# Performance work log

Measured on AMD Instinct MI355X. Metric: run time of the kernel, lower is better.

## Reference

```python
import jax, jax.numpy as jnp
import numpy as np

# dims: T time steps, B batch, CIN/COUT conv channels, HxW spatial, K kernel
T, B, CIN, COUT, H, Wd, K = 10, 32, 3, 64, 64, 64, 3
DECAY = 0.2      # LIF leak factor
INH = 1.625      # lateral inhibition strength (mode='threshold')


def setup_inputs() -> dict:
    key = jax.random.key(0)
    k1, k2 = jax.random.split(key)
    x = (jax.random.uniform(k1, (T, B, CIN, H, Wd)) < 0.2).astype(jnp.float32)
    W = jax.random.normal(k2, (COUT, CIN, K, K), dtype=jnp.float32)
    # normweight(): zero-mean, unit-std (biased) per output filter
    W = W - W.mean(axis=(1, 2, 3), keepdims=True)
    W = W / W.reshape(COUT, -1).std(axis=1).reshape(COUT, 1, 1, 1)
    return {"x": x, "W": W}


def _conv(x, W):
    # Conv2d stride=1, padding=1, no bias, NCHW/OIHW
    return jax.lax.conv_general_dilated(
        x, W, window_strides=(1, 1), padding=((1, 1), (1, 1)),
        dimension_numbers=("NCHW", "OIHW", "NCHW"))


def reference(x, W):
    def step(mem, x_t):
        i = _conv(x_t, W)                                        # (B,COUT,H,W)
        # ATB: adaptive per-channel threshold = max over batch+spatial
        thr = jnp.max(i, axis=(0, 2, 3), keepdims=True) + 1e-4   # (1,COUT,1,1)
        # ASF: clamp then thresholded sigmoid filter
        cur = jnp.maximum(i, 0.0)
        i_asf = thr * jax.nn.sigmoid((cur - 0.4 * thr) * (8.0 / thr))
        # LIF update with threshold = thr (set by ATB)
        mem = mem * DECAY + i_asf
        s = (mem > thr).astype(mem.dtype)                        # spikes 0/1
        # WTA k=1: keep only the strongest spiking channel per location
        score = mem * s
        winner = jnp.argmax(score, axis=1)                       # (B,H,W)
        oh = jnp.moveaxis(jax.nn.one_hot(winner, COUT, dtype=mem.dtype), -1, 1)
        s = s * oh
        # membrane reset of fired neurons
        mem = mem * (1.0 - s)
        # lateral inhibition: suppress non-winners at spiking locations
        any_sp = jnp.max(s, axis=1, keepdims=True)
        mem = mem - INH * thr * any_sp * (1.0 - s)
        return mem, s

    mem0 = jnp.zeros((B, COUT, H, Wd), jnp.float32)
    _, spikes = jax.lax.scan(step, mem0, x)
    return spikes  # (T,B,COUT,H,W)
```

## Files before the change

kernel.cpp:

```cpp
#include <hip/hip_runtime.h>
#include <math.h>

#define TT 10
#define BB 32
#define CIN 3
#define COUT 64
#define HH 64
#define WW 64
#define HW (HH*WW)
#define DECAY 0.2f
#define INH 1.625f

__device__ __forceinline__ unsigned int enc_f(float f) {
    unsigned int u = __float_as_uint(f);
    return (u & 0x80000000u) ? ~u : (u | 0x80000000u);
}
__device__ __forceinline__ float dec_f(unsigned int u) {
    u = (u & 0x80000000u) ? (u & 0x7FFFFFFFu) : ~u;
    return __uint_as_float(u);
}

__global__ __launch_bounds__(256) void thr_kernel(
    const float* __restrict__ x,
    const float* __restrict__ Wt,
    unsigned int* __restrict__ thr_raw)
{
    __shared__ float sx[CIN][6][68];
    __shared__ float wmax[4][COUT];

    const int tid  = threadIdx.x;
    const int lane = tid & 63;
    const int wave = tid >> 6;
    const int h0   = blockIdx.x * 4;
    const int b    = blockIdx.y;
    const int t    = blockIdx.z;

    float w[27];
    #pragma unroll
    for (int k = 0; k < 27; k++) w[k] = Wt[lane * 27 + k];

    const float* xb = x + ((size_t)t * BB + b) * (CIN * HW);
    for (int l = tid; l < CIN * 6 * 66; l += 256) {
        int ci  = l / 396;
        int r   = (l % 396) / 66;
        int col = l % 66;
        int gh = h0 + r - 1;
        int gw = col - 1;
        float v = 0.f;
        if (gh >= 0 && gh < HH && gw >= 0 && gw < WW)
            v = xb[ci * HW + gh * WW + gw];
        sx[ci][r][col] = v;
    }
    __syncthreads();

    float mx = -INFINITY;

    for (int cc = 0; cc < 16; cc++) {
        float acc0 = 0.f, acc1 = 0.f, acc2 = 0.f, acc3 = 0.f;
        #pragma unroll
        for (int ci = 0; ci < CIN; ci++)
            #pragma unroll
            for (int kh = 0; kh < 3; kh++) {
                const float* rp = &sx[ci][wave + kh][cc * 4];
                float4 q = *(const float4*)rp;
                float2 r2 = *(const float2*)(rp + 4);
                float x0 = q.x, x1 = q.y, x2 = q.z, x3 = q.w;
                float x4 = r2.x, x5 = r2.y;
                const float w0 = w[ci * 9 + kh * 3 + 0];
                const float w1 = w[ci * 9 + kh * 3 + 1];
                const float w2 = w[ci * 9 + kh * 3 + 2];
                acc0 = fmaf(w0, x0, acc0); acc0 = fmaf(w1, x1, acc0); acc0 = fmaf(w2, x2, acc0);
                acc1 = fmaf(w0, x1, acc1); acc1 = fmaf(w1, x2, acc1); acc1 = fmaf(w2, x3, acc1);
                acc2 = fmaf(w0, x2, acc2); acc2 = fmaf(w1, x3, acc2); acc2 = fmaf(w2, x4, acc2);
                acc3 = fmaf(w0, x3, acc3); acc3 = fmaf(w1, x4, acc3); acc3 = fmaf(w2, x5, acc3);
            }
        mx = fmaxf(mx, fmaxf(fmaxf(acc0, acc1), fmaxf(acc2, acc3)));
    }

    wmax[wave][lane] = mx;
    __syncthreads();
    if (wave == 0) {
        float m = fmaxf(fmaxf(wmax[0][lane], wmax[1][lane]),
                        fmaxf(wmax[2][lane], wmax[3][lane]));
        atomicMax(&thr_raw[t * COUT + lane], enc_f(m));
    }
}

__global__ __launch_bounds__(256) void fused_kernel(
    const float* __restrict__ x,
    const float* __restrict__ Wt,
    const unsigned int* __restrict__ thr_raw,
    float* __restrict__ out)
{
    __shared__ float sx[CIN][3][68];

    const int tid  = threadIdx.x;
    const int lane = tid & 63;
    const int wave = tid >> 6;
    const int p0   = __builtin_amdgcn_readfirstlane(wave * 16);
    const int b    = blockIdx.x >> 6;
    const int h    = blockIdx.x & 63;

    float w[27];
    #pragma unroll
    for (int k = 0; k < 27; k++) w[k] = Wt[lane * 27 + k];

    float mem[16];
    #pragma unroll
    for (int j = 0; j < 16; j++) mem[j] = 0.f;

    #pragma unroll 1
    for (int t = 0; t < TT; t++) {
        const float* xb = x + ((size_t)t * BB + b) * (CIN * HW);
        for (int l = tid; l < CIN * 3 * 66; l += 256) {
            int ci  = l / 198;
            int r   = (l % 198) / 66;
            int col = l % 66;
            int gh = h + r - 1;
            int gw = col - 1;
            float v = 0.f;
            if (gh >= 0 && gh < HH && gw >= 0 && gw < WW)
                v = xb[ci * HW + gh * WW + gw];
            sx[ci][r][col] = v;
        }

        float* os = out + (((size_t)t * BB + b) * COUT) * HW + h * WW;

        #pragma unroll
        for (int g = 0; g < 4; g++) {
            int c  = g * 16 + (tid >> 4);
            int w4 = (tid & 15) * 4;
            *(float4*)(os + (size_t)c * HW + w4) = make_float4(0.f, 0.f, 0.f, 0.f);
        }

        __syncthreads();

        float thr   = dec_f(thr_raw[t * COUT + lane]) + 1e-4f;
        float sinv  = 8.0f / thr;
        float s04   = 0.4f * thr;
        float sinh_ = INH * thr;

        int fmask = 0;

#define LIF_PX(J, ACC) {                                                    \
        float cur = fmaxf(ACC, 0.f);                                        \
        float z   = (cur - s04) * sinv;                                     \
        float sig = 1.0f / (1.0f + expf(-z));                               \
        float m   = mem[J] * DECAY + thr * sig;                             \
        int   sp  = m > thr;                                                \
        float score = sp ? m : 0.f;                                         \
        unsigned long long blt = __ballot(sp);                              \
        int fr = 0, sp_any = 0;                                             \
        if (blt) {                                  \
            float bs = score;                                               \
            int   bc = lane;                                                \
            _Pragma("unroll")                                               \
            for (int off = 32; off > 0; off >>= 1) {                        \
                float so = __shfl_xor(bs, off, 64);                         \
                int   co = __shfl_xor(bc, off, 64);                         \
                if (so > bs || (so == bs && co < bc)) { bs = so; bc = co; } \
            }                                                               \
            int spw = __shfl(sp, bc, 64);      \
            fr     = (lane == bc) && sp;                                    \
            sp_any = spw;                                                   \
        }                                                                   \
        mem[J] = fr ? 0.f : (m - (sp_any ? sinh_ : 0.f));                   \
        if (fr) fmask |= (1 << (J));                                        \
    }

        #pragma unroll
        for (int ch = 0; ch < 4; ch++) {
            const int c0 = p0 + ch * 4;
            float acc0 = 0.f, acc1 = 0.f, acc2 = 0.f, acc3 = 0.f;
            #pragma unroll
            for (int ci = 0; ci < CIN; ci++)
                #pragma unroll
                for (int kh = 0; kh < 3; kh++) {
                    const float* rp = &sx[ci][kh][c0];
                    float4 q = *(const float4*)rp;
                    float2 r2 = *(const float2*)(rp + 4);
                    float x0 = q.x, x1 = q.y, x2 = q.z, x3 = q.w;
                    float x4 = r2.x, x5 = r2.y;
                    const float w0 = w[ci * 9 + kh * 3 + 0];
                    const float w1 = w[ci * 9 + kh * 3 + 1];
                    const float w2 = w[ci * 9 + kh * 3 + 2];
                    acc0 = fmaf(w0, x0, acc0); acc0 = fmaf(w1, x1, acc0); acc0 = fmaf(w2, x2, acc0);
                    acc1 = fmaf(w0, x1, acc1); acc1 = fmaf(w1, x2, acc1); acc1 = fmaf(w2, x3, acc1);
                    acc2 = fmaf(w0, x2, acc2); acc2 = fmaf(w1, x3, acc2); acc2 = fmaf(w2, x4, acc2);
                    acc3 = fmaf(w0, x3, acc3); acc3 = fmaf(w1, x4, acc3); acc3 = fmaf(w2, x5, acc3);
                }
            LIF_PX(ch * 4 + 0, acc0);
            LIF_PX(ch * 4 + 1, acc1);
            LIF_PX(ch * 4 + 2, acc2);
            LIF_PX(ch * 4 + 3, acc3);
        }
#undef LIF_PX

        if (fmask) {
            #pragma unroll
            for (int j = 0; j < 16; j++)
                if (fmask & (1 << j))
                    os[(size_t)lane * HW + p0 + j] = 1.0f;
        }
        __syncthreads();
    }
}

extern "C" void kernel_launch(void* const* d_in, const int* in_sizes, int n_in,
                              void* d_out, int out_size, void* d_ws, size_t ws_size,
                              hipStream_t stream) {
    const float* x = (const float*)d_in[0];
    const float* W = (const float*)d_in[1];
    float* out     = (float*)d_out;

    unsigned int* thr = (unsigned int*)d_ws;
    hipMemsetAsync(thr, 0, TT * COUT * sizeof(unsigned int), stream);

    thr_kernel<<<dim3(HH / 4, BB, TT), 256, 0, stream>>>(x, W, thr);
    fused_kernel<<<dim3(BB * HH), 256, 0, stream>>>(x, W, thr, out);
}
```

Baseline: 532.6 us.

## Preload all time steps' input tiles and zero outputs before the time loop

The fused kernel now loads the padded input rows for all 10 time steps into shared memory at once (about 24KB per block) and zeroes all output rows up front. This removes the per-timestep global load and the two barriers in each iteration of the serial time loop, so that latency is exposed only once. It also sets a minimum of 6 blocks per SM in the launch bounds. The larger shared-memory footprint and the register cap may limit occupancy or cause spills.

```diff
diff --git a/kernel.cpp b/kernel.cpp
--- a/kernel.cpp
+++ b/kernel.cpp
@@ -86,13 +86,13 @@
     }
 }
 
-__global__ __launch_bounds__(256) void fused_kernel(
+__global__ __launch_bounds__(256, 6) void fused_kernel(
     const float* __restrict__ x,
     const float* __restrict__ Wt,
     const unsigned int* __restrict__ thr_raw,
     float* __restrict__ out)
 {
-    __shared__ float sx[CIN][3][68];
+    __shared__ float sx[TT][CIN][3][68];
 
     const int tid  = threadIdx.x;
     const int lane = tid & 63;
@@ -105,40 +105,52 @@
     #pragma unroll
     for (int k = 0; k < 27; k++) w[k] = Wt[lane * 27 + k];
 
-    float mem[16];
-    #pragma unroll
-    for (int j = 0; j < 16; j++) mem[j] = 0.f;
-
-    #pragma unroll 1
-    for (int t = 0; t < TT; t++) {
-        const float* xb = x + ((size_t)t * BB + b) * (CIN * HW);
-        for (int l = tid; l < CIN * 3 * 66; l += 256) {
-            int ci  = l / 198;
-            int r   = (l % 198) / 66;
-            int col = l % 66;
+    {
+        const float* xb0 = x + (size_t)b * (CIN * HW);
+        for (int l = tid; l < TT * CIN * 3 * 66; l += 256) {
+            int t   = l / 594;
+            int r0  = l - t * 594;
+            int ci  = r0 / 198;
+            int r1  = r0 - ci * 198;
+            int r   = r1 / 66;
+            int col = r1 - r * 66;
             int gh = h + r - 1;
             int gw = col - 1;
             float v = 0.f;
             if (gh >= 0 && gh < HH && gw >= 0 && gw < WW)
-                v = xb[ci * HW + gh * WW + gw];
-            sx[ci][r][col] = v;
-        }
-
-        float* os = out + (((size_t)t * BB + b) * COUT) * HW + h * WW;
-
+                v = xb0[(size_t)t * ((size_t)BB * CIN * HW) + ci * HW + gh * WW + gw];
+            sx[t][ci][r][col] = v;
+        }
+    }
+
+    {
+        float* os0 = out + ((size_t)b * COUT) * HW + h * WW;
         #pragma unroll
-        for (int g = 0; g < 4; g++) {
-            int c  = g * 16 + (tid >> 4);
-            int w4 = (tid & 15) * 4;
-            *(float4*)(os + (size_t)c * HW + w4) = make_float4(0.f, 0.f, 0.f, 0.f);
-        }
-
-        __syncthreads();
-
+        for (int t = 0; t < TT; t++) {
+            float* os = os0 + (size_t)t * ((size_t)BB * COUT * HW);
+            #pragma unroll
+            for (int g = 0; g < 4; g++) {
+                int c  = g * 16 + (tid >> 4);
+                int w4 = (tid & 15) * 4;
+                *(float4*)(os + (size_t)c * HW + w4) = make_float4(0.f, 0.f, 0.f, 0.f);
+            }
+        }
+    }
+
+    float mem[16];
+    #pragma unroll
+    for (int j = 0; j < 16; j++) mem[j] = 0.f;
+
+    __syncthreads();
+
+    #pragma unroll 1
+    for (int t = 0; t < TT; t++) {
         float thr   = dec_f(thr_raw[t * COUT + lane]) + 1e-4f;
         float sinv  = 8.0f / thr;
         float s04   = 0.4f * thr;
         float sinh_ = INH * thr;
+
+        float* os = out + (((size_t)t * BB + b) * COUT) * HW + h * WW;
 
         int fmask = 0;
 
@@ -176,7 +188,7 @@
             for (int ci = 0; ci < CIN; ci++)
                 #pragma unroll
                 for (int kh = 0; kh < 3; kh++) {
-                    const float* rp = &sx[ci][kh][c0];
+                    const float* rp = &sx[t][ci][kh][c0];
                     float4 q = *(const float4*)rp;
                     float2 r2 = *(const float2*)(rp + 4);
                     float x0 = q.x, x1 = q.y, x2 = q.z, x3 = q.w;
@@ -202,7 +214,6 @@
                 if (fmask & (1 << j))
                     os[(size_t)lane * HW + p0 + j] = 1.0f;
         }
-        __syncthreads();
     }
 }
 
```

Result: slower. 909.5 us (+70.8%).

## Stage five timesteps of input at once and write spikes with one float4 pass

Applied to the files above, without the earlier changes.

The fused kernel now loads input halo rows for five timesteps into a larger shared buffer in one go, which cuts the per-timestep load-then-barrier pattern down to two staging phases. The separate zero-fill pass plus the scattered writes of spike ones are replaced by a single pass: each wave shuffles the per-channel fire masks so that every lane builds and stores one float4 of 0/1 values for its channel. A minimum-occupancy hint is added to the launch bounds. In exchange the shared memory per block is about five times larger, which may limit how many blocks fit on each compute unit.

```diff
diff --git a/kernel.cpp b/kernel.cpp
--- a/kernel.cpp
+++ b/kernel.cpp
@@ -86,13 +86,13 @@
     }
 }
 
-__global__ __launch_bounds__(256) void fused_kernel(
+__global__ __launch_bounds__(256, 8) void fused_kernel(
     const float* __restrict__ x,
     const float* __restrict__ Wt,
     const unsigned int* __restrict__ thr_raw,
     float* __restrict__ out)
 {
-    __shared__ float sx[CIN][3][68];
+    __shared__ float sx[5][CIN][3][68];
 
     const int tid  = threadIdx.x;
     const int lane = tid & 63;
@@ -105,35 +105,42 @@
     #pragma unroll
     for (int k = 0; k < 27; k++) w[k] = Wt[lane * 27 + k];
 
+    const float* xb0 = x + (size_t)b * (CIN * HW);
+
+#define STAGE5(T0) {                                                          \
+        for (int l = tid; l < 5 * 594; l += 256) {                            \
+            int t   = l / 594;                                                \
+            int r0  = l - t * 594;                                            \
+            int ci  = r0 / 198;                                               \
+            int r1  = r0 - ci * 198;                                          \
+            int r   = r1 / 66;                                                \
+            int col = r1 - r * 66;                                            \
+            int gh = h + r - 1;                                               \
+            int gw = col - 1;                                                 \
+            float v = 0.f;                                                    \
+            if (gh >= 0 && gh < HH && gw >= 0 && gw < WW)                     \
+                v = xb0[(size_t)((T0) + t) * ((size_t)BB * CIN * HW)          \
+                        + ci * HW + gh * WW + gw];                            \
+            sx[t][ci][r][col] = v;                                            \
+        }                                                                     \
+    }
+
+    STAGE5(0);
+
     float mem[16];
     #pragma unroll
     for (int j = 0; j < 16; j++) mem[j] = 0.f;
 
+    __syncthreads();
+
     #pragma unroll 1
     for (int t = 0; t < TT; t++) {
-        const float* xb = x + ((size_t)t * BB + b) * (CIN * HW);
-        for (int l = tid; l < CIN * 3 * 66; l += 256) {
-            int ci  = l / 198;
-            int r   = (l % 198) / 66;
-            int col = l % 66;
-            int gh = h + r - 1;
-            int gw = col - 1;
-            float v = 0.f;
-            if (gh >= 0 && gh < HH && gw >= 0 && gw < WW)
-                v = xb[ci * HW + gh * WW + gw];
-            sx[ci][r][col] = v;
+        if (t == 5) {
+            __syncthreads();
+            STAGE5(5);
+            __syncthreads();
         }
-
-        float* os = out + (((size_t)t * BB + b) * COUT) * HW + h * WW;
-
-        #pragma unroll
-        for (int g = 0; g < 4; g++) {
-            int c  = g * 16 + (tid >> 4);
-            int w4 = (tid & 15) * 4;
-            *(float4*)(os + (size_t)c * HW + w4) = make_float4(0.f, 0.f, 0.f, 0.f);
-        }
-
-        __syncthreads();
+        const int slot = (t < 5) ? t : t - 5;
 
         float thr   = dec_f(thr_raw[t * COUT + lane]) + 1e-4f;
         float sinv  = 8.0f / thr;
@@ -176,7 +183,7 @@
             for (int ci = 0; ci < CIN; ci++)
                 #pragma unroll
                 for (int kh = 0; kh < 3; kh++) {
-                    const float* rp = &sx[ci][kh][c0];
+                    const float* rp = &sx[slot][ci][kh][c0];
                     float4 q = *(const float4*)rp;
                     float2 r2 = *(const float2*)(rp + 4);
                     float x0 = q.x, x1 = q.y, x2 = q.z, x3 = q.w;
@@ -196,14 +203,22 @@
         }
 #undef LIF_PX
 
-        if (fmask) {
-            #pragma unroll
-            for (int j = 0; j < 16; j++)
-                if (fmask & (1 << j))
-                    os[(size_t)lane * HW + p0 + j] = 1.0f;
+        float* os = out + (((size_t)t * BB + b) * COUT) * HW + h * WW;
+        #pragma unroll
+        for (int k = 0; k < 4; k++) {
+            const int c   = k * 16 + (lane >> 2);
+            const int pix = (lane & 3) * 4;
+            int fm  = __shfl(fmask, c, 64);
+            int nib = (fm >> pix) & 0xF;
+            float4 v;
+            v.x = (nib & 1) ? 1.f : 0.f;
+            v.y = (nib & 2) ? 1.f : 0.f;
+            v.z = (nib & 4) ? 1.f : 0.f;
+            v.w = (nib & 8) ? 1.f : 0.f;
+            *(float4*)(os + (size_t)c * HW + p0 + pix) = v;
         }
-        __syncthreads();
-    }
+    }
+#undef STAGE5
 }
 
 extern "C" void kernel_launch(void* const* d_in, const int* in_sizes, int n_in,
```

New measurement: 2.028 ms. +280.8%, slower.
